# Kernel tuning notes

Measured on AMD Instinct MI355X. Metric: run time of the kernel, lower is better.

## Reference

```python
import jax, jax.numpy as jnp
import numpy as np

_SAMPLING_EPS = 1e-5
BIG_NEG = jnp.float32(-1e30)  # finite stand-in for -inf (exact 0 after softmax in fp32)


def setup_inputs() -> dict:
    key = jax.random.key(0)
    ks = jax.random.split(key, 12)
    B, V, P, O, S = 128, 128000, 2048, 256, 4
    return {
        "logits": jax.random.normal(ks[0], (B, V), jnp.float32) * 4.0,
        "prompt_token_ids": jax.random.randint(ks[1], (B, P), 0, V),
        "output_token_ids": jax.random.randint(ks[2], (B, O), 0, V),
        "stop_token_ids": jax.random.randint(ks[3], (B, S), 0, V),
        "min_tokens": jax.random.randint(ks[4], (B,), 0, 512),
        "presence_penalties": jax.random.uniform(ks[5], (B,), jnp.float32),
        "frequency_penalties": jax.random.uniform(ks[6], (B,), jnp.float32),
        "repetition_penalties": 1.0 + 0.3 * jax.random.uniform(ks[7], (B,), jnp.float32),
        "temperature": 0.5 + jax.random.uniform(ks[8], (B,), jnp.float32),
        "top_k": jax.random.randint(ks[9], (B,), 32, 64),
        "top_p": 0.5 + 0.5 * jax.random.uniform(ks[10], (B,), jnp.float32),
        "uniform_noise": jax.random.uniform(ks[11], (B, V), jnp.float32, minval=1e-10, maxval=1.0),
        "max_num_logprobs": 20,
    }


def reference(logits, prompt_token_ids, output_token_ids, stop_token_ids,
              min_tokens, presence_penalties, frequency_penalties,
              repetition_penalties, temperature, top_k, top_p,
              uniform_noise, max_num_logprobs):
    B, V = logits.shape
    x = logits.astype(jnp.float32)
    rows = jnp.arange(B)[:, None]

    # ---- min-token penalty: set stop-token logits to -inf while len(output) < min_tokens
    need = min_tokens > output_token_ids.shape[1]                  # [B]
    stop_pen = jnp.where(need[:, None], BIG_NEG, jnp.inf)          # [B,S]
    x = x.at[rows, stop_token_ids].min(stop_pen)

    # ---- presence / frequency / repetition penalties (vLLM apply_penalties)
    counts = jnp.zeros((B, V), jnp.float32).at[rows, output_token_ids].add(1.0)
    prompt_mask = jnp.zeros((B, V), bool).at[rows, prompt_token_ids].set(True)
    output_mask = counts > 0
    rp = repetition_penalties[:, None]
    penalized = jnp.where(x > 0, x / rp, x * rp)
    x = jnp.where(prompt_mask | output_mask, penalized, x)
    x = x - frequency_penalties[:, None] * counts \
          - presence_penalties[:, None] * output_mask.astype(jnp.float32)

    # ---- temperature (greedy rows: temp treated as 1.0)
    t = jnp.where(temperature < _SAMPLING_EPS, 1.0, temperature)
    x = x / t[:, None]

    # ---- top-k / top-p filtering (per-row k and p)
    order = jnp.argsort(-x, axis=-1)                               # descending
    srt = jnp.take_along_axis(x, order, axis=-1)
    pos = jnp.arange(V)[None, :]
    k_eff = jnp.where(top_k < 1, V, top_k)
    keep_k = pos < k_eff[:, None]
    probs_s = jax.nn.softmax(srt, axis=-1)
    cum = jnp.cumsum(probs_s, axis=-1)
    keep_p = (cum - probs_s) < top_p[:, None]                      # cumulative mass before token < p
    keep = jnp.zeros((B, V), bool).at[rows, order].set(keep_k & keep_p)
    x = jnp.where(keep, x, BIG_NEG)

    orig_logits = x
    # source applies temperature a second time before the final sample
    x2 = x / t[:, None]

    # ---- sample: Gumbel-max random sampling, greedy where temperature ~ 0
    gumbel = -jnp.log(-jnp.log(uniform_noise))
    random_sampled = jnp.argmax(x2 + gumbel, axis=-1)
    greedy_sampled = jnp.argmax(x2, axis=-1)
    sampled = jnp.where(temperature < _SAMPLING_EPS, greedy_sampled,
                        random_sampled).astype(jnp.int32)

    # ---- top-k logprobs
    logprobs = jax.nn.log_softmax(orig_logits, axis=-1)
    topk_logprobs, topk_indices = jax.lax.top_k(logprobs, max_num_logprobs)
    return sampled, topk_logprobs, topk_indices.astype(jnp.int32)
```

## Files before the change

kernel.cpp:

```cpp
#include <hip/hip_runtime.h>
#include <math.h>

#define VV 128000
#define NB 128
#define PP 2048
#define OO 256

#define S   8
#define CH  16000
#define CW  500
#define NT1 512
#define CAP 512
#define HS1 512

#define NT2 256

#define BIG_NEG_F (-1e30f)
#define PAD_KEY 0x007FFFFF80000000ULL
#define LOG2E 1.4426950408889634f

__device__ __forceinline__ unsigned long long packkey(float f, int idx) {
  unsigned int b = __float_as_uint(f);
  unsigned int mf = (b & 0x80000000u) ? ~b : (b | 0x80000000u);
  return ((unsigned long long)mf << 32) | (unsigned long long)(unsigned int)(~(unsigned int)idx);
}
__device__ __forceinline__ float unpack_val(unsigned long long k) {
  unsigned int mf = (unsigned int)(k >> 32);
  unsigned int b = (mf & 0x80000000u) ? (mf & 0x7fffffffu) : ~mf;
  return __uint_as_float(b);
}
__device__ __forceinline__ int unpack_idx(unsigned long long k) {
  return (int)(~(unsigned int)(k & 0xffffffffu));
}
__device__ __forceinline__ float ulp_down(float f, int n) {
  unsigned int b = __float_as_uint(f);
  unsigned int m = (b & 0x80000000u) ? ~b : (b | 0x80000000u);
  m -= (unsigned int)n;
  unsigned int r = (m & 0x80000000u) ? (m & 0x7fffffffu) : ~m;
  return __uint_as_float(r);
}

__device__ __forceinline__ float wave_sort64_desc(float v, int lane) {
  for (int k = 2; k <= 64; k <<= 1) {
    for (int j = k >> 1; j > 0; j >>= 1) {
      float o = __shfl_xor(v, j, 64);
      bool smaller = (lane & j) == 0;
      bool dir = (lane & k) == 0;
      v = (smaller == dir) ? fmaxf(v, o) : fminf(v, o);
    }
  }
  return v;
}
__device__ __forceinline__ unsigned long long wave_sort64_desc_u64(unsigned long long v, int lane) {
  for (int k = 2; k <= 64; k <<= 1) {
    for (int j = k >> 1; j > 0; j >>= 1) {
      unsigned long long o = __shfl_xor(v, j, 64);
      bool smaller = (lane & j) == 0;
      bool dir = (lane & k) == 0;
      unsigned long long mx = (v > o) ? v : o;
      unsigned long long mn = (v > o) ? o : v;
      v = (smaller == dir) ? mx : mn;
    }
  }
  return v;
}
__device__ __forceinline__ unsigned long long merge_top64(unsigned long long v,
                                                          const unsigned long long* B,
                                                          int lane) {
  unsigned long long b = B[63 - lane];
  v = (v > b) ? v : b;
  for (int j = 32; j > 0; j >>= 1) {
    unsigned long long o = __shfl_xor(v, j, 64);
    bool hi = (lane & j) == 0;
    unsigned long long mx = (v > o) ? v : o;
    unsigned long long mn = (v > o) ? o : v;
    v = hi ? mx : mn;
  }
  return v;
}

__global__ __launch_bounds__(NT1)
void k_main(const float* __restrict__ logits,
            const int* __restrict__ prompt_ids,
            const int* __restrict__ output_ids,
            const int* __restrict__ stop_ids,
            const int* __restrict__ min_tokens,
            const float* __restrict__ presence_p,
            const float* __restrict__ frequency_p,
            const float* __restrict__ repetition_p,
            const float* __restrict__ temperature,
            float* __restrict__ ws_sum,
            unsigned long long* __restrict__ ws_top)
{
#pragma clang fp contract(off)
  __shared__ unsigned int pbits[CW];
  __shared__ unsigned int obits[CW];
  __shared__ int hkey[HS1];
  __shared__ int hval[HS1];
  __shared__ unsigned long long cand[CAP];
  __shared__ unsigned long long mbuf[4 * 64];
  __shared__ float wtau[NT1 / 64];
  __shared__ float wsum[NT1 / 64];
  __shared__ float tau_sh;
  __shared__ int cnt_sh;

  const int chunk = blockIdx.x;
  const int row   = blockIdx.y;
  const int tid   = threadIdx.x;
  const int lane  = tid & 63;
  const int wv    = tid >> 6;
  const int base  = chunk * CH;

  const float fp  = frequency_p[row];
  const float pp  = presence_p[row];
  const float rp  = repetition_p[row];
  const float inv_rp = 1.0f / rp;
  const float tmp = temperature[row];
  const float t   = (tmp < 1e-5f) ? 1.0f : tmp;
  const float c2  = LOG2E / t;
  const bool need = min_tokens[row] > OO;
  const int s0 = stop_ids[row * 4 + 0];
  const int s1 = stop_ids[row * 4 + 1];
  const int s2 = stop_ids[row * 4 + 2];
  const int s3 = stop_ids[row * 4 + 3];
  const bool anystop = need &&
      (((unsigned)(s0 - base) < CH) || ((unsigned)(s1 - base) < CH) ||
       ((unsigned)(s2 - base) < CH) || ((unsigned)(s3 - base) < CH));

  for (int i = tid; i < CW; i += NT1) { pbits[i] = 0u; obits[i] = 0u; }
  for (int i = tid; i < HS1; i += NT1) { hkey[i] = -1; hval[i] = 0; }
  if (tid == 0) cnt_sh = 0;
  __syncthreads();

  const int4* pr4 = (const int4*)(prompt_ids + (size_t)row * PP);
  for (int i = tid; i < PP / 4; i += NT1) {
    int4 tv = pr4[i];
    int l;
    l = tv.x - base; if ((unsigned)l < CH) atomicOr(&pbits[l >> 5], 1u << (l & 31));
    l = tv.y - base; if ((unsigned)l < CH) atomicOr(&pbits[l >> 5], 1u << (l & 31));
    l = tv.z - base; if ((unsigned)l < CH) atomicOr(&pbits[l >> 5], 1u << (l & 31));
    l = tv.w - base; if ((unsigned)l < CH) atomicOr(&pbits[l >> 5], 1u << (l & 31));
  }
  for (int i = tid; i < OO; i += NT1) {
    int tok = output_ids[row * OO + i];
    int l = tok - base;
    if ((unsigned)l < CH) {
      atomicOr(&obits[l >> 5], 1u << (l & 31));
      unsigned int h = ((unsigned int)tok * 2654435761u) >> 23;
      for (;;) {
        int k = hkey[h];
        if (k == tok) { atomicAdd(&hval[h], 1); break; }
        if (k == -1) {
          int prev = atomicCAS(&hkey[h], -1, tok);
          if (prev == -1 || prev == tok) { atomicAdd(&hval[h], 1); break; }
          continue;
        }
        h = (h + 1) & (HS1 - 1);
      }
    }
  }
  __syncthreads();

  const float* __restrict__ lrow = logits + (size_t)row * VV + base;
  const int l0 = (0 * NT1 + tid) << 3;
  const int l1 = (1 * NT1 + tid) << 3;
  const int l2 = (2 * NT1 + tid) << 3;
  const int l3 = (3 * NT1 + tid) << 3;
  const bool v3 = l3 < CH;

  unsigned int stopmask = 0u;
  if (anystop) {
    const int sids[4] = {s0, s1, s2, s3};
#pragma unroll
    for (int q = 0; q < 4; ++q) {
      int local = sids[q] - base;
      if ((unsigned)local < CH) {
        int grp = (local >> 3) / NT1;
        int tt  = (local >> 3) % NT1;
        if (tt == tid) stopmask |= 1u << (grp * 8 + (local & 7));
      }
    }
  }

  float4 A0 = *(const float4*)(lrow + l0);
  float4 B0 = *(const float4*)(lrow + l0 + 4);
  float4 A1 = *(const float4*)(lrow + l1);
  float4 B1 = *(const float4*)(lrow + l1 + 4);
  float4 A2 = *(const float4*)(lrow + l2);
  float4 B2 = *(const float4*)(lrow + l2 + 4);
  float4 A3, B3;
  if (v3) { A3 = *(const float4*)(lrow + l3); B3 = *(const float4*)(lrow + l3 + 4); }

  float gm0 = -INFINITY, gm1 = -INFINITY, gm2 = -INFINITY, gm3 = -INFINITY;
  float esum = 0.0f;

  auto processA = [&](int li, float4 xa, float4 xb, float& gm, unsigned int sm8) {
    unsigned int w  = (unsigned)li >> 5;
    unsigned int sh = (unsigned)li & 31u;
    unsigned int pm8 = (pbits[w] >> sh) & 255u;
    unsigned int om8 = (obits[w] >> sh) & 255u;
    float xs[8] = {xa.x, xa.y, xa.z, xa.w, xb.x, xb.y, xb.z, xb.w};
    if (sm8) {
#pragma unroll
      for (int e = 0; e < 8; ++e)
        if ((sm8 >> e) & 1u) xs[e] = BIG_NEG_F;
    }
#pragma unroll
    for (int e = 0; e < 8; ++e) {
      float xp = xs[e];
      if ((pm8 | om8) & (1u << e)) {
        xp = (xp > 0.0f) ? (xp * inv_rp) : (xp * rp);
        if ((om8 >> e) & 1u) {
          int v = base + li + e;
          float cnt = 0.0f;
          unsigned int h = ((unsigned int)v * 2654435761u) >> 23;
          for (;;) {
            int k = hkey[h];
            if (k == -1) break;
            if (k == v) { cnt = (float)hval[h]; break; }
            h = (h + 1) & (HS1 - 1);
          }
          xp = xp - fp * cnt - pp;
        }
      }
      gm = fmaxf(gm, xp);
      esum += exp2f(xp * c2);
    }
  };

  processA(l0, A0, B0, gm0, stopmask & 255u);
  processA(l1, A1, B1, gm1, (stopmask >> 8) & 255u);
  processA(l2, A2, B2, gm2, (stopmask >> 16) & 255u);
  if (v3) processA(l3, A3, B3, gm3, (stopmask >> 24) & 255u);

  float mx = fmaxf(fmaxf(gm0, gm1), fmaxf(gm2, gm3));

  float ss = esum;
#pragma unroll
  for (int off = 32; off > 0; off >>= 1) ss += __shfl_down(ss, off, 64);
  if (lane == 0) wsum[wv] = ss;

  float srt = wave_sort64_desc(mx, lane);
  if (lane == 7) wtau[wv] = srt;
  __syncthreads();

  if (tid == 0) {
    float tau = wtau[0];
#pragma unroll
    for (int w = 1; w < NT1 / 64; ++w) tau = fminf(tau, wtau[w]);
    tau_sh = ulp_down(tau, 16);
    float sacc = 0.0f;
#pragma unroll
    for (int w = 0; w < NT1 / 64; ++w) sacc += wsum[w];
    ws_sum[row * S + chunk] = sacc;
  }
  __syncthreads();
  const float taueff = tau_sh;

  auto processB = [&](int li, float gmv) {
    if (gmv < taueff) return;
    float4 xa = *(const float4*)(lrow + li);
    float4 xb = *(const float4*)(lrow + li + 4);
    float xs[8] = {xa.x, xa.y, xa.z, xa.w, xb.x, xb.y, xb.z, xb.w};
#pragma unroll
    for (int e = 0; e < 8; ++e) {
      float x = xs[e];
      if (x >= taueff) {
        int v = base + li + e;
        int ll = li + e;
        if (anystop && ((v == s0) | (v == s1) | (v == s2) | (v == s3)))
          x = fminf(x, BIG_NEG_F);
        bool pm = (pbits[(unsigned)ll >> 5] >> ((unsigned)ll & 31u)) & 1u;
        bool om = (obits[(unsigned)ll >> 5] >> ((unsigned)ll & 31u)) & 1u;
        float cnt = 0.0f;
        if (om) {
          unsigned int h = ((unsigned int)v * 2654435761u) >> 23;
          for (;;) {
            int k = hkey[h];
            if (k == -1) break;
            if (k == v) { cnt = (float)hval[h]; break; }
            h = (h + 1) & (HS1 - 1);
          }
        }
        if (pm || om) x = (x > 0.0f) ? (x / rp) : (x * rp);
        x = x - fp * cnt;
        if (om) x = x - pp;
        if (x >= taueff) {
          float xd = x / t;
          int p = atomicAdd(&cnt_sh, 1);
          if (p < CAP) cand[p] = packkey(xd, v);
        }
      }
    }
  };

  processB(l0, gm0);
  processB(l1, gm1);
  processB(l2, gm2);
  if (v3) processB(l3, gm3);

  __syncthreads();
  int total = cnt_sh; if (total > CAP) total = CAP;
  for (int i = tid; i < CAP; i += NT1)
    if (i >= total) cand[i] = PAD_KEY;
  __syncthreads();

  unsigned long long rv = wave_sort64_desc_u64(cand[(wv << 6) + lane], lane);
  cand[(wv << 6) + lane] = rv;
  __syncthreads();

  if (wv < 4) {
    unsigned long long a = cand[((2 * wv) << 6) + lane];
    a = merge_top64(a, &cand[(2 * wv + 1) << 6], lane);
    mbuf[(wv << 6) + lane] = a;
  }
  __syncthreads();
  if (wv < 2) {
    unsigned long long a = mbuf[((2 * wv) << 6) + lane];
    a = merge_top64(a, &mbuf[(2 * wv + 1) << 6], lane);
    cand[(wv << 6) + lane] = a;
  }
  __syncthreads();
  if (wv == 0) {
    unsigned long long a = cand[lane];
    a = merge_top64(a, &cand[64], lane);
    ws_top[((size_t)row * S + chunk) * 64 + lane] = a;
  }
}

__global__ __launch_bounds__(NT2)
void k2_finalize(const float* __restrict__ temperature,
                 const int* __restrict__ top_k,
                 const float* __restrict__ top_p,
                 const float* __restrict__ noise,
                 const unsigned long long* __restrict__ ws_top,
                 const float* __restrict__ ws_sum,
                 float* __restrict__ out, int K)
{
#pragma clang fp contract(off)
  __shared__ unsigned long long buf[S * 64];
  __shared__ unsigned long long mbuf[4 * 64];
  __shared__ float sv[64];
  __shared__ int   si[64];
  __shared__ float se[64];
  __shared__ float gv[64];

  const int row  = blockIdx.x;
  const int tid  = threadIdx.x;
  const int lane = tid & 63;
  const int wv   = tid >> 6;

  const float tmp = temperature[row];
  const float t   = (tmp < 1e-5f) ? 1.0f : tmp;
  const int   tk  = top_k[row];
  const float tpv = top_p[row];

  for (int i = tid; i < S * 64; i += NT2)
    buf[i] = ws_top[(size_t)row * S * 64 + i];
  __syncthreads();

  {
    unsigned long long a = buf[((2 * wv) << 6) + lane];
    a = merge_top64(a, &buf[(2 * wv + 1) << 6], lane);
    mbuf[(wv << 6) + lane] = a;
  }
  __syncthreads();
  if (wv < 2) {
    unsigned long long a = mbuf[((2 * wv) << 6) + lane];
    a = merge_top64(a, &mbuf[(2 * wv + 1) << 6], lane);
    buf[(wv << 6) + lane] = a;
  }
  __syncthreads();
  if (wv == 0) {
    unsigned long long a = buf[lane];
    a = merge_top64(a, &buf[64], lane);
    float val = unpack_val(a);
    int   idx = unpack_idx(a);
    float m = __shfl(val, 0, 64);
    sv[lane] = val;
    si[lane] = idx;
    bool ok = (unsigned)idx < VV;
    float u = ok ? noise[(size_t)row * VV + idx] : 0.5f;
    float g = -logf(-logf(u));
    se[lane] = expf(val - m);
    gv[lane] = val / t + g;
  }
  __syncthreads();

  if (tid == 0) {
    float Ssum = 0.0f;
    for (int c = 0; c < S; c++) Ssum += ws_sum[row * S + c];
    const float m = sv[0];
    const float Z = Ssum * exp2f(-m * LOG2E);

    int keff = (tk < 1) ? 64 : (tk < 64 ? tk : 64);

    float cum = 0.0f;
    int nk = 0;
    for (int j = 0; j < 64; j++) {
      if (j >= keff) break;
      if (!(cum < tpv)) break;
      nk++;
      cum += se[j] / Z;
    }

    float Zk = 0.0f;
    for (int j = 0; j < nk; j++) Zk += se[j];
    const float logZk = logf(Zk);

    float bv = -INFINITY; int bi = 0x7fffffff;
    for (int j = 0; j < nk; j++) {
      float val = gv[j];
      if (val > bv || (val == bv && si[j] < bi)) { bv = val; bi = si[j]; }
    }
    const int samp = (tmp < 1e-5f) ? si[0] : bi;
    out[row] = (float)samp;

    unsigned long long bm0 = 0ull, bm1 = 0ull;
    for (int j = 0; j < nk; j++) {
      int ix = si[j];
      if (ix < 64) bm0 |= 1ull << ix;
      else if (ix < 128) bm1 |= 1ull << (ix - 64);
    }
    int fi = 0;
    for (int j = 0; j < K; j++) {
      float lp; int ix;
      if (j < nk) {
        lp = (sv[j] - m) - logZk;
        ix = si[j];
      } else {
        while ((fi < 64) ? ((bm0 >> fi) & 1ull) : ((bm1 >> (fi - 64)) & 1ull)) fi++;
        ix = fi; fi++;
        lp = BIG_NEG_F;
      }
      out[NB + row * K + j]            = lp;
      out[NB + NB * K + row * K + j]   = (float)ix;
    }
  }
}

extern "C" void kernel_launch(void* const* d_in, const int* in_sizes, int n_in,
                              void* d_out, int out_size, void* d_ws, size_t ws_size,
                              hipStream_t stream) {
  const float* logits = (const float*)d_in[0];
  const int*   prompt = (const int*)d_in[1];
  const int*   outids = (const int*)d_in[2];
  const int*   stop   = (const int*)d_in[3];
  const int*   mint   = (const int*)d_in[4];
  const float* pres   = (const float*)d_in[5];
  const float* freq   = (const float*)d_in[6];
  const float* rep    = (const float*)d_in[7];
  const float* temp   = (const float*)d_in[8];
  const int*   topk   = (const int*)d_in[9];
  const float* topp   = (const float*)d_in[10];
  const float* noise  = (const float*)d_in[11];

  int B_ = in_sizes[4];
  int K_ = (out_size - B_) / (2 * B_);

  float* ws_sum = (float*)d_ws;
  unsigned long long* ws_top = (unsigned long long*)(ws_sum + (size_t)NB * S);

  dim3 g1(S, B_);
  k_main<<<g1, NT1, 0, stream>>>(logits, prompt, outids, stop, mint,
                                 pres, freq, rep, temp, ws_sum, ws_top);
  k2_finalize<<<B_, NT2, 0, stream>>>(temp, topk, topp, noise,
                                      ws_top, ws_sum, (float*)d_out, K_);
}
```

Baseline: 196.8 us.

## Keep penalized logits in registers, prefetch before histogram build, adaptive merge depth

Logit loads are issued before the prompt/output bitmap and hash-table construction so global latency overlaps the shared-memory setup. The penalized values from the first pass are kept in per-thread register arrays and reused in the candidate pass, so the second global reload and the repeated penalty and hash lookups are gone. The tau slack is removed because the candidate values are now computed exactly, and the sort/merge tree skips waves and levels when few candidates exist. A launch-bounds occupancy hint is added; the 32 extra live floats per thread raise register pressure, which may cause spills.

New measurement: 196.3 us. About the same (-0.2%).

```diff
diff --git a/kernel.cpp b/kernel.cpp
--- a/kernel.cpp
+++ b/kernel.cpp
@@ -31,13 +31,6 @@
 }
 __device__ __forceinline__ int unpack_idx(unsigned long long k) {
   return (int)(~(unsigned int)(k & 0xffffffffu));
-}
-__device__ __forceinline__ float ulp_down(float f, int n) {
-  unsigned int b = __float_as_uint(f);
-  unsigned int m = (b & 0x80000000u) ? ~b : (b | 0x80000000u);
-  m -= (unsigned int)n;
-  unsigned int r = (m & 0x80000000u) ? (m & 0x7fffffffu) : ~m;
-  return __uint_as_float(r);
 }
 
 __device__ __forceinline__ float wave_sort64_desc(float v, int lane) {
@@ -79,7 +72,7 @@
   return v;
 }
 
-__global__ __launch_bounds__(NT1)
+__global__ __launch_bounds__(NT1, 4)
 void k_main(const float* __restrict__ logits,
             const int* __restrict__ prompt_ids,
             const int* __restrict__ output_ids,
@@ -127,6 +120,22 @@
       (((unsigned)(s0 - base) < CH) || ((unsigned)(s1 - base) < CH) ||
        ((unsigned)(s2 - base) < CH) || ((unsigned)(s3 - base) < CH));
 
+  const float* __restrict__ lrow = logits + (size_t)row * VV + base;
+  const int l0 = (0 * NT1 + tid) << 3;
+  const int l1 = (1 * NT1 + tid) << 3;
+  const int l2 = (2 * NT1 + tid) << 3;
+  const int l3 = (3 * NT1 + tid) << 3;
+  const bool v3 = l3 < CH;
+
+  float4 A0 = *(const float4*)(lrow + l0);
+  float4 B0 = *(const float4*)(lrow + l0 + 4);
+  float4 A1 = *(const float4*)(lrow + l1);
+  float4 B1 = *(const float4*)(lrow + l1 + 4);
+  float4 A2 = *(const float4*)(lrow + l2);
+  float4 B2 = *(const float4*)(lrow + l2 + 4);
+  float4 A3, B3;
+  if (v3) { A3 = *(const float4*)(lrow + l3); B3 = *(const float4*)(lrow + l3 + 4); }
+
   for (int i = tid; i < CW; i += NT1) { pbits[i] = 0u; obits[i] = 0u; }
   for (int i = tid; i < HS1; i += NT1) { hkey[i] = -1; hval[i] = 0; }
   if (tid == 0) cnt_sh = 0;
@@ -159,14 +168,6 @@
       }
     }
   }
-  __syncthreads();
-
-  const float* __restrict__ lrow = logits + (size_t)row * VV + base;
-  const int l0 = (0 * NT1 + tid) << 3;
-  const int l1 = (1 * NT1 + tid) << 3;
-  const int l2 = (2 * NT1 + tid) << 3;
-  const int l3 = (3 * NT1 + tid) << 3;
-  const bool v3 = l3 < CH;
 
   unsigned int stopmask = 0u;
   if (anystop) {
@@ -181,20 +182,14 @@
       }
     }
   }
-
-  float4 A0 = *(const float4*)(lrow + l0);
-  float4 B0 = *(const float4*)(lrow + l0 + 4);
-  float4 A1 = *(const float4*)(lrow + l1);
-  float4 B1 = *(const float4*)(lrow + l1 + 4);
-  float4 A2 = *(const float4*)(lrow + l2);
-  float4 B2 = *(const float4*)(lrow + l2 + 4);
-  float4 A3, B3;
-  if (v3) { A3 = *(const float4*)(lrow + l3); B3 = *(const float4*)(lrow + l3 + 4); }
-
+  __syncthreads();
+
+  float px0[8], px1[8], px2[8], px3[8];
   float gm0 = -INFINITY, gm1 = -INFINITY, gm2 = -INFINITY, gm3 = -INFINITY;
   float esum = 0.0f;
 
-  auto processA = [&](int li, float4 xa, float4 xb, float& gm, unsigned int sm8) {
+  auto processA = [&](int li, float4 xa, float4 xb, float (&px)[8],
+                      float& gm, unsigned int sm8) {
     unsigned int w  = (unsigned)li >> 5;
     unsigned int sh = (unsigned)li & 31u;
     unsigned int pm8 = (pbits[w] >> sh) & 255u;
@@ -208,8 +203,10 @@
 #pragma unroll
     for (int e = 0; e < 8; ++e) {
       float xp = xs[e];
+      float xe = xp;
       if ((pm8 | om8) & (1u << e)) {
-        xp = (xp > 0.0f) ? (xp * inv_rp) : (xp * rp);
+        float xa_ = (xp > 0.0f) ? (xp * inv_rp) : (xp * rp);
+        float xd_ = (xp > 0.0f) ? (xp / rp)     : (xp * rp);
         if ((om8 >> e) & 1u) {
           int v = base + li + e;
           float cnt = 0.0f;
@@ -220,18 +217,23 @@
             if (k == v) { cnt = (float)hval[h]; break; }
             h = (h + 1) & (HS1 - 1);
           }
-          xp = xp - fp * cnt - pp;
+          xa_ = xa_ - fp * cnt - pp;
+          xd_ = xd_ - fp * cnt - pp;
         }
+        esum += exp2f(xa_ * c2);
+        xe = xd_;
+      } else {
+        esum += exp2f(xp * c2);
       }
-      gm = fmaxf(gm, xp);
-      esum += exp2f(xp * c2);
+      gm = fmaxf(gm, xe);
+      px[e] = xe;
     }
   };
 
-  processA(l0, A0, B0, gm0, stopmask & 255u);
-  processA(l1, A1, B1, gm1, (stopmask >> 8) & 255u);
-  processA(l2, A2, B2, gm2, (stopmask >> 16) & 255u);
-  if (v3) processA(l3, A3, B3, gm3, (stopmask >> 24) & 255u);
+  processA(l0, A0, B0, px0, gm0, stopmask & 255u);
+  processA(l1, A1, B1, px1, gm1, (stopmask >> 8) & 255u);
+  processA(l2, A2, B2, px2, gm2, (stopmask >> 16) & 255u);
+  if (v3) processA(l3, A3, B3, px3, gm3, (stopmask >> 24) & 255u);
 
   float mx = fmaxf(fmaxf(gm0, gm1), fmaxf(gm2, gm3));
 
@@ -248,7 +250,7 @@
     float tau = wtau[0];
 #pragma unroll
     for (int w = 1; w < NT1 / 64; ++w) tau = fminf(tau, wtau[w]);
-    tau_sh = ulp_down(tau, 16);
+    tau_sh = tau;
     float sacc = 0.0f;
 #pragma unroll
     for (int w = 0; w < NT1 / 64; ++w) sacc += wsum[w];
@@ -257,47 +259,23 @@
   __syncthreads();
   const float taueff = tau_sh;
 
-  auto processB = [&](int li, float gmv) {
+  auto processB = [&](int li, const float (&px)[8], float gmv) {
     if (gmv < taueff) return;
-    float4 xa = *(const float4*)(lrow + li);
-    float4 xb = *(const float4*)(lrow + li + 4);
-    float xs[8] = {xa.x, xa.y, xa.z, xa.w, xb.x, xb.y, xb.z, xb.w};
 #pragma unroll
     for (int e = 0; e < 8; ++e) {
-      float x = xs[e];
-      if (x >= taueff) {
-        int v = base + li + e;
-        int ll = li + e;
-        if (anystop && ((v == s0) | (v == s1) | (v == s2) | (v == s3)))
-          x = fminf(x, BIG_NEG_F);
-        bool pm = (pbits[(unsigned)ll >> 5] >> ((unsigned)ll & 31u)) & 1u;
-        bool om = (obits[(unsigned)ll >> 5] >> ((unsigned)ll & 31u)) & 1u;
-        float cnt = 0.0f;
-        if (om) {
-          unsigned int h = ((unsigned int)v * 2654435761u) >> 23;
-          for (;;) {
-            int k = hkey[h];
-            if (k == -1) break;
-            if (k == v) { cnt = (float)hval[h]; break; }
-            h = (h + 1) & (HS1 - 1);
-          }
-        }
-        if (pm || om) x = (x > 0.0f) ? (x / rp) : (x * rp);
-        x = x - fp * cnt;
-        if (om) x = x - pp;
-        if (x >= taueff) {
-          float xd = x / t;
-          int p = atomicAdd(&cnt_sh, 1);
-          if (p < CAP) cand[p] = packkey(xd, v);
-        }
+      float xe = px[e];
+      if (xe >= taueff) {
+        float xd = xe / t;
+        int p = atomicAdd(&cnt_sh, 1);
+        if (p < CAP) cand[p] = packkey(xd, base + li + e);
       }
     }
   };
 
-  processB(l0, gm0);
-  processB(l1, gm1);
-  processB(l2, gm2);
-  if (v3) processB(l3, gm3);
+  processB(l0, px0, gm0);
+  processB(l1, px1, gm1);
+  processB(l2, px2, gm2);
+  if (v3) processB(l3, px3, gm3);
 
   __syncthreads();
   int total = cnt_sh; if (total > CAP) total = CAP;
@@ -305,26 +283,52 @@
     if (i >= total) cand[i] = PAD_KEY;
   __syncthreads();
 
-  unsigned long long rv = wave_sort64_desc_u64(cand[(wv << 6) + lane], lane);
-  cand[(wv << 6) + lane] = rv;
-  __syncthreads();
-
-  if (wv < 4) {
-    unsigned long long a = cand[((2 * wv) << 6) + lane];
-    a = merge_top64(a, &cand[(2 * wv + 1) << 6], lane);
-    mbuf[(wv << 6) + lane] = a;
-  }
-  __syncthreads();
-  if (wv < 2) {
-    unsigned long long a = mbuf[((2 * wv) << 6) + lane];
-    a = merge_top64(a, &mbuf[(2 * wv + 1) << 6], lane);
-    cand[(wv << 6) + lane] = a;
-  }
-  __syncthreads();
-  if (wv == 0) {
-    unsigned long long a = cand[lane];
-    a = merge_top64(a, &cand[64], lane);
-    ws_top[((size_t)row * S + chunk) * 64 + lane] = a;
+  int runs = (total + 63) >> 6; if (runs < 1) runs = 1;
+  if (wv < runs) {
+    unsigned long long rv = wave_sort64_desc_u64(cand[(wv << 6) + lane], lane);
+    cand[(wv << 6) + lane] = rv;
+  }
+  __syncthreads();
+
+  unsigned long long* outp = &ws_top[((size_t)row * S + chunk) * 64 + lane];
+  if (runs > 4) {
+    if (wv < 4) {
+      unsigned long long a = cand[((2 * wv) << 6) + lane];
+      a = merge_top64(a, &cand[(2 * wv + 1) << 6], lane);
+      mbuf[(wv << 6) + lane] = a;
+    }
+    __syncthreads();
+    if (wv < 2) {
+      unsigned long long a = mbuf[((2 * wv) << 6) + lane];
+      a = merge_top64(a, &mbuf[(2 * wv + 1) << 6], lane);
+      cand[(wv << 6) + lane] = a;
+    }
+    __syncthreads();
+    if (wv == 0) {
+      unsigned long long a = cand[lane];
+      a = merge_top64(a, &cand[64], lane);
+      *outp = a;
+    }
+  } else if (runs > 2) {
+    if (wv < 2) {
+      unsigned long long a = cand[((2 * wv) << 6) + lane];
+      a = merge_top64(a, &cand[(2 * wv + 1) << 6], lane);
+      mbuf[(wv << 6) + lane] = a;
+    }
+    __syncthreads();
+    if (wv == 0) {
+      unsigned long long a = mbuf[lane];
+      a = merge_top64(a, &mbuf[64], lane);
+      *outp = a;
+    }
+  } else if (runs == 2) {
+    if (wv == 0) {
+      unsigned long long a = cand[lane];
+      a = merge_top64(a, &cand[64], lane);
+      *outp = a;
+    }
+  } else {
+    if (wv == 0) *outp = cand[lane];
   }
 }
 
```
